# Performance work log

Measured on AMD Instinct MI355X. Metric: run time of the kernel, lower is better.

The kernel has to match this reference:

```python
import jax, jax.numpy as jnp
import numpy as np
import math

VOCAB = 32000
HIDDEN = 256
N_HEADS = 8
HEAD_DIM = 32
MAX_LEN = 2048


def _pos_encoding(max_len, d_model, dtype=jnp.float32):
    # Matches PositionalEncoding buffer (even d_model).
    pos = jnp.arange(max_len, dtype=dtype)[:, None]                       # [L,1]
    div = jnp.exp(jnp.arange(0, d_model, 2, dtype=dtype) * (-(math.log(10000.0) / d_model)))
    ang = pos * div                                                        # [L, d/2]
    pe = jnp.zeros((max_len, d_model), dtype=dtype)
    pe = pe.at[:, 0::2].set(jnp.sin(ang))
    pe = pe.at[:, 1::2].set(jnp.cos(ang))
    return pe


def setup_inputs() -> dict:
    key = jax.random.key(0)
    ks = jax.random.split(key, 7)
    B, S = 8, 2047
    s = 0.02
    x = jax.random.randint(ks[0], (B, S), 0, VOCAB + 1, dtype=jnp.int64)
    emb_w = jax.random.normal(ks[1], (VOCAB + 1, HIDDEN), jnp.float32) * s
    wq = jax.random.normal(ks[2], (N_HEADS, HEAD_DIM, HIDDEN), jnp.float32) * s
    wk = jax.random.normal(ks[3], (N_HEADS, HEAD_DIM, HIDDEN), jnp.float32) * s
    wv = jax.random.normal(ks[4], (N_HEADS, HEAD_DIM, HIDDEN), jnp.float32) * s
    wo = jax.random.normal(ks[5], (HIDDEN, N_HEADS * HEAD_DIM), jnp.float32) * s
    wu = jax.random.normal(ks[6], (VOCAB + 1, HIDDEN), jnp.float32) * s
    return {"x": x, "emb_w": emb_w, "wq": wq, "wk": wk, "wv": wv, "wo": wo, "wu": wu}


def reference(x, emb_w, wq, wk, wv, wo, wu):
    B, S = x.shape
    # prepend CLS token (id=2)
    tok = jnp.concatenate([jnp.full((B, 1), 2, dtype=x.dtype), x], axis=1)  # [B, S+1]
    y = emb_w[tok]                                                          # [B, S+1, H]
    y = y + _pos_encoding(S + 1, HIDDEN, y.dtype)
    # batched per-head QKV (nn.Linear: out = in @ W.T)
    q = jnp.einsum('bsh,nkh->bnsk', y, wq)
    k = jnp.einsum('bsh,nkh->bnsk', y, wk)
    v = jnp.einsum('bsh,nkh->bnsk', y, wv)
    scores = jnp.einsum('bnsk,bntk->bnst', q, k) / (HEAD_DIM ** 0.5)        # [B,N,S+1,S+1]
    A = jax.nn.softmax(scores, axis=-1)
    o = jnp.einsum('bnst,bntk->bnsk', A, v)                                 # [B,N,S+1,K]
    o = jnp.transpose(o, (0, 2, 1, 3)).reshape(B, S + 1, N_HEADS * HEAD_DIM)
    att = o @ wo.T + y     # residual inside MultiHeadAttention
    y = att + y            # second residual in MultiHeadTransformerPosEmb.forward
    out = y[:, 0, :] @ wu.T                                                 # [B, VOCAB+1]
    return out
```

## Files before the change

### kernel.cpp

```cpp
#include <hip/hip_runtime.h>
#include <stdint.h>

#define B_   8
#define S_   2047
#define L_   2048
#define H_   256
#define NH_  8
#define HD_  32
#define V_   32001
#define NCH_ 128
#define TCH_ 16
#define GRID_ 1024
#define BAR_STRIDE_ 2048

__device__ __forceinline__ void ast(float* p, float v) {
    __hip_atomic_store((unsigned int*)p, __float_as_uint(v),
                       __ATOMIC_RELAXED, __HIP_MEMORY_SCOPE_AGENT);
}
__device__ __forceinline__ float ald(const float* p) {
    return __uint_as_float(__hip_atomic_load((const unsigned int*)p,
                           __ATOMIC_RELAXED, __HIP_MEMORY_SCOPE_AGENT));
}
__device__ __forceinline__ unsigned aadd(unsigned* p) {
    return __hip_atomic_fetch_add(p, 1u, __ATOMIC_RELAXED, __HIP_MEMORY_SCOPE_AGENT);
}
__device__ __forceinline__ unsigned aldu(const unsigned* p) {
    return __hip_atomic_load(p, __ATOMIC_RELAXED, __HIP_MEMORY_SCOPE_AGENT);
}
__device__ __forceinline__ void vdrain() {
    asm volatile("s_waitcnt vmcnt(0)" ::: "memory");
}
__device__ __forceinline__ float foldx(float a, int off) {
    return a + __shfl_xor(a, off, 64);
}
__device__ __forceinline__ float sel8(const float a[8], int j) {
    float v = a[0];
    v = (j == 1) ? a[1] : v;
    v = (j == 2) ? a[2] : v;
    v = (j == 3) ? a[3] : v;
    v = (j == 4) ? a[4] : v;
    v = (j == 5) ? a[5] : v;
    v = (j == 6) ? a[6] : v;
    v = (j == 7) ? a[7] : v;
    return v;
}

__global__ __launch_bounds__(256, 4) void mega(const int* __restrict__ x,
                                               const float* __restrict__ emb,
                                               const float* __restrict__ wq,
                                               const float* __restrict__ wk,
                                               const float* __restrict__ wv,
                                               const float* __restrict__ wo,
                                               const float* __restrict__ wu,
                                               float* __restrict__ out,
                                               float* __restrict__ qk,
                                               float* __restrict__ z,
                                               float* __restrict__ obar,
                                               float* __restrict__ ebar,
                                               unsigned int* __restrict__ bars) {
    int bid = blockIdx.x, tid = threadIdx.x;

    __shared__ float smem[4][2056];
    float* smf = &smem[0][0];

    unsigned* qbar = bars;
    unsigned* acnt = bars + BAR_STRIDE_;
    unsigned* zbar = bars + 2 * BAR_STRIDE_;

    if (bid < NH_) {
        int n = bid;
        float* y0l = smem[0];
        float* q0p = smem[1];
        float* q0l = smem[2];
        float v = emb[2 * H_ + tid] + ((tid & 1) ? 1.0f : 0.0f);
        y0l[tid] = v;
        __syncthreads();
        {
            int k = tid >> 3, part = tid & 7;
            const float* w = wq + (n * HD_ + k) * H_ + part * 32;
            const float* yy = y0l + part * 32;
            float acc = 0.f;
#pragma unroll
            for (int j = 0; j < 32; ++j) acc += w[j] * yy[j];
            q0p[k * 8 + part] = acc;
        }
        __syncthreads();
        if (tid < HD_) {
            float s = 0.f;
#pragma unroll
            for (int j = 0; j < 8; ++j) s += q0p[tid * 8 + j];
            q0l[tid] = s;
        }
        __syncthreads();
        float acc = 0.f;
        for (int k = 0; k < HD_; ++k)
            acc += q0l[k] * wk[(n * HD_ + k) * H_ + tid];
        ast(qk + n * H_ + tid, acc * 0.17677669529663687f);
        vdrain();
        __syncthreads();
        if (tid == 0) {
            if (aadd(qbar) == NH_ - 1) {
                for (int i = 0; i < 32; ++i)
                    __hip_atomic_store(qbar + 528 + i * 16, 1u,
                                       __ATOMIC_RELAXED, __HIP_MEMORY_SCOPE_AGENT);
            }
        }
        __syncthreads();
    }

    {
        int b = bid >> 7, c = bid & 127;
        int lane = tid & 63, w = tid >> 6;
        int h0 = lane * 4;
        int t0 = c * TCH_ + w * 4;

        int toks[4];
#pragma unroll
        for (int i = 0; i < 4; ++i) {
            int t = t0 + i;
            toks[i] = (t == 0) ? 2 : x[b * S_ + t - 1];
        }
        float4 evr[4];
#pragma unroll
        for (int i = 0; i < 4; ++i)
            evr[i] = *(const float4*)(emb + (size_t)toks[i] * H_ + h0);
        const float cdiv = 0.07195578414202881f;
        float div0 = __expf(-(float)(lane * 2) * cdiv);
        float div1 = __expf(-(float)(lane * 2 + 1) * cdiv);
        __builtin_amdgcn_sched_barrier(0);

        if (tid == 0) {
            while (aldu(qbar + 528 + (bid & 31) * 16) == 0u)
                __builtin_amdgcn_s_sleep(2);
        }
        __syncthreads();

        for (int i = tid; i < NH_ * H_; i += 256)
            smem[3][i] = ald(qk + i);
        __syncthreads();
        float4 qr[NH_];
#pragma unroll
        for (int n = 0; n < NH_; ++n)
            qr[n] = *(const float4*)&smem[3][n * H_ + h0];
        __syncthreads();

        float4 acc[NH_];
        float es[NH_];
#pragma unroll
        for (int n = 0; n < NH_; ++n) {
            acc[n] = make_float4(0.f, 0.f, 0.f, 0.f);
            es[n] = 0.f;
        }

#pragma unroll
        for (int i = 0; i < 4; ++i) {
            int t = t0 + i;
            float4 ev = evr[i];
            float a0 = (float)t * div0, a1 = (float)t * div1;
            float4 y4;
            y4.x = ev.x + __sinf(a0); y4.y = ev.y + __cosf(a0);
            y4.z = ev.z + __sinf(a1); y4.w = ev.w + __cosf(a1);

            float a[NH_];
#pragma unroll
            for (int n = 0; n < NH_; ++n)
                a[n] = qr[n].x * y4.x + qr[n].y * y4.y + qr[n].z * y4.z + qr[n].w * y4.w;

            float m4[4];
#pragma unroll
            for (int k = 0; k < 4; ++k) {
                float lo = foldx(a[k], 32), hi = foldx(a[k + 4], 32);
                m4[k] = (lane & 32) ? hi : lo;
            }
            float m2[2];
#pragma unroll
            for (int k = 0; k < 2; ++k) {
                float lo = foldx(m4[k], 16), hi = foldx(m4[k + 2], 16);
                m2[k] = (lane & 16) ? hi : lo;
            }
            float lo = foldx(m2[0], 8), hi = foldx(m2[1], 8);
            float m1 = (lane & 8) ? hi : lo;
            m1 = foldx(m1, 4); m1 = foldx(m1, 2); m1 = foldx(m1, 1);
            float e = __expf(m1);

#pragma unroll
            for (int n = 0; n < NH_; ++n) {
                float en = __shfl(e, n * 8, 64);
                acc[n].x += en * y4.x; acc[n].y += en * y4.y;
                acc[n].z += en * y4.z; acc[n].w += en * y4.w;
                es[n] += en;
            }
        }

#pragma unroll
        for (int n = 0; n < NH_; ++n)
            *(float4*)&smem[w][n * H_ + h0] = acc[n];
        if (lane < NH_) smem[w][2048 + lane] = sel8(es, lane);
        __syncthreads();

#pragma unroll
        for (int jj = 0; jj < (NH_ * H_) / 256; ++jj) {
            int j = jj * 256 + tid;
            atomicAdd(obar + b * (NH_ * H_) + j,
                      smem[0][j] + smem[1][j] + smem[2][j] + smem[3][j]);
        }
        if (tid < NH_)
            atomicAdd(ebar + b * NH_ + tid,
                      smem[0][2048 + tid] + smem[1][2048 + tid]
                    + smem[2][2048 + tid] + smem[3][2048 + tid]);
        vdrain();
        __syncthreads();
        if (tid == 0) aadd(acnt);
    }

    if (bid >= 8 && bid < 16) {
        int b = bid - 8;
        if (tid == 0) {
            while (aldu(acnt) < (unsigned)GRID_) __builtin_amdgcn_s_sleep(2);
        }
        __syncthreads();
        float* ybar_l = smf;
        float* o_l    = smf + 2048;
        float* sB     = smf + 2304;
        if (tid < NH_) sB[tid] = 1.0f / ald(ebar + b * NH_ + tid);
        __syncthreads();
        for (int i = tid; i < NH_ * H_; i += 256)
            ybar_l[i] = ald(obar + b * (NH_ * H_) + i) * sB[i >> 8];
        __syncthreads();
        {
            int n = tid >> 5;
            const float* wrow = wv + (size_t)tid * H_;
            const float* yy = ybar_l + n * H_;
            float s = 0.f;
#pragma unroll 16
            for (int j4 = 0; j4 < H_ / 4; ++j4) {
                float4 w4 = *(const float4*)(wrow + j4 * 4);
                s += w4.x * yy[j4 * 4] + w4.y * yy[j4 * 4 + 1]
                   + w4.z * yy[j4 * 4 + 2] + w4.w * yy[j4 * 4 + 3];
            }
            o_l[tid] = s;
        }
        __syncthreads();
        {
            float y0v = emb[2 * H_ + tid] + ((tid & 1) ? 1.0f : 0.0f);
            const float* wrow = wo + (size_t)tid * (NH_ * HD_);
            float s = 0.f;
#pragma unroll 16
            for (int j4 = 0; j4 < (NH_ * HD_) / 4; ++j4) {
                float4 w4 = *(const float4*)(wrow + j4 * 4);
                s += w4.x * o_l[j4 * 4] + w4.y * o_l[j4 * 4 + 1]
                   + w4.z * o_l[j4 * 4 + 2] + w4.w * o_l[j4 * 4 + 3];
            }
            ast(z + b * H_ + tid, s + 2.0f * y0v);
        }
        vdrain();
        __syncthreads();
        if (tid == 0) {
            if (aadd(zbar) == B_ - 1) {
                for (int i = 0; i < 32; ++i)
                    __hip_atomic_store(zbar + 528 + i * 16, 1u,
                                       __ATOMIC_RELAXED, __HIP_MEMORY_SCOPE_AGENT);
            }
        }
        __syncthreads();
    }

    {
        int lane = tid & 63, w = tid >> 6;
        int m = lane & 15, g = lane >> 4;
        int base = bid * 32;

        int rl0 = w * 4 + g;
        int v0 = base + rl0;
        int vc0 = (v0 < V_) ? v0 : (V_ - 1);
        const float* wr0 = wu + (size_t)vc0 * H_ + m * 16;
        float4 p00 = *(const float4*)(wr0);
        float4 p01 = *(const float4*)(wr0 + 4);
        float4 p02 = *(const float4*)(wr0 + 8);
        float4 p03 = *(const float4*)(wr0 + 12);
        __builtin_amdgcn_sched_barrier(0);

        if (tid == 0) {
            while (aldu(zbar + 528 + (bid & 31) * 16) == 0u)
                __builtin_amdgcn_s_sleep(2);
        }
        __syncthreads();

        float* zs = smf;
        float* sm_out = smf + 2560;
        for (int i = tid; i < B_ * H_; i += 256) {
            int bb = i >> 8, h = i & 255;
            zs[bb * 320 + (h >> 4) * 20 + (h & 15)] = ald(z + i);
        }
        __syncthreads();

#pragma unroll
        for (int pass = 0; pass < 2; ++pass) {
            int rl = pass * 16 + w * 4 + g;
            float4 w0, w1, w2, w3;
            if (pass == 0) { w0 = p00; w1 = p01; w2 = p02; w3 = p03; }
            else {
                int v = base + rl;
                int vc = (v < V_) ? v : (V_ - 1);
                const float* wr = wu + (size_t)vc * H_ + m * 16;
                w0 = *(const float4*)(wr);
                w1 = *(const float4*)(wr + 4);
                w2 = *(const float4*)(wr + 8);
                w3 = *(const float4*)(wr + 12);
            }
            float acc[B_];
#pragma unroll
            for (int bb = 0; bb < B_; ++bb) {
                const float* zb = zs + bb * 320 + m * 20;
                float4 z0 = *(const float4*)(zb);
                float4 z1 = *(const float4*)(zb + 4);
                float4 z2 = *(const float4*)(zb + 8);
                float4 z3 = *(const float4*)(zb + 12);
                acc[bb] = z0.x * w0.x + z0.y * w0.y + z0.z * w0.z + z0.w * w0.w
                        + z1.x * w1.x + z1.y * w1.y + z1.z * w1.z + z1.w * w1.w
                        + z2.x * w2.x + z2.y * w2.y + z2.z * w2.z + z2.w * w2.w
                        + z3.x * w3.x + z3.y * w3.y + z3.z * w3.z + z3.w * w3.w;
            }
#pragma unroll
            for (int off = 1; off <= 8; off <<= 1) {
#pragma unroll
                for (int bb = 0; bb < B_; ++bb) acc[bb] += __shfl_xor(acc[bb], off, 64);
            }
            if (m < B_) sm_out[m * 33 + rl] = sel8(acc, m);
        }
        __syncthreads();
        {
            int bb = tid >> 5, vl = tid & 31, vv = base + vl;
            if (vv < V_) out[bb * V_ + vv] = sm_out[bb * 33 + vl];
        }
    }
}

extern "C" void kernel_launch(void* const* d_in, const int* in_sizes, int n_in,
                              void* d_out, int out_size, void* d_ws, size_t ws_size,
                              hipStream_t stream) {
    const int*   x   = (const int*)d_in[0];
    const float* emb = (const float*)d_in[1];
    const float* wq  = (const float*)d_in[2];
    const float* wk  = (const float*)d_in[3];
    const float* wv  = (const float*)d_in[4];
    const float* wo  = (const float*)d_in[5];
    const float* wu  = (const float*)d_in[6];
    float*       out = (float*)d_out;

    float* qk   = (float*)d_ws;
    float* z    = qk + NH_ * H_;
    float* obar = z + B_ * H_;
    float* ebar = obar + B_ * NH_ * H_;
    unsigned int* bars = (unsigned int*)(ebar + B_ * NH_);

    hipMemsetAsync(obar, 0,
                   (B_ * NH_ * H_ + B_ * NH_) * sizeof(float)
                 + 3 * BAR_STRIDE_ * sizeof(unsigned int), stream);

    mega<<<GRID_, 256, 0, stream>>>(x, emb, wq, wk, wv, wo, wu, out,
                                    qk, z, obar, ebar, bars);
}
```

Measured before the change: 160.7 us.

## Replace contended atomic reduction with partial-sum buffers and replicate broadcast vectors

Each attention block now writes its per-block partial sums to a private psum slot instead of doing float atomicAdds into a shared obar. A new grid-wide reduction stage of 512 blocks, gated by an extra barrier, sums those partials. The qk and z broadcast vectors are written as 64 replicas so readers spread across different addresses, and the ebar counters are padded to separate cache lines. The aim is to cut atomic contention and hot-spot reads, at the cost of an extra barrier phase and more global traffic.

```diff
diff --git a/kernel.cpp b/kernel.cpp
--- a/kernel.cpp
+++ b/kernel.cpp
@@ -11,6 +11,7 @@
 #define NCH_ 128
 #define TCH_ 16
 #define GRID_ 1024
+#define NREP_ 64
 #define BAR_STRIDE_ 2048
 
 __device__ __forceinline__ void ast(float* p, float v) {
@@ -53,10 +54,11 @@
                                                const float* __restrict__ wo,
                                                const float* __restrict__ wu,
                                                float* __restrict__ out,
-                                               float* __restrict__ qk,
-                                               float* __restrict__ z,
+                                               float* __restrict__ qk_rep,
+                                               float* __restrict__ z_rep,
+                                               float* __restrict__ psum,
                                                float* __restrict__ obar,
-                                               float* __restrict__ ebar,
+                                               float* __restrict__ ebar_pad,
                                                unsigned int* __restrict__ bars) {
     int bid = blockIdx.x, tid = threadIdx.x;
 
@@ -64,8 +66,9 @@
     float* smf = &smem[0][0];
 
     unsigned* qbar = bars;
-    unsigned* acnt = bars + BAR_STRIDE_;
-    unsigned* zbar = bars + 2 * BAR_STRIDE_;
+    unsigned* abar = bars + BAR_STRIDE_;
+    unsigned* rbar = bars + 2 * BAR_STRIDE_;
+    unsigned* zbar = bars + 3 * BAR_STRIDE_;
 
     if (bid < NH_) {
         int n = bid;
@@ -95,7 +98,9 @@
         float acc = 0.f;
         for (int k = 0; k < HD_; ++k)
             acc += q0l[k] * wk[(n * HD_ + k) * H_ + tid];
-        ast(qk + n * H_ + tid, acc * 0.17677669529663687f);
+        float qv = acc * 0.17677669529663687f;
+        for (int r = 0; r < NREP_; ++r)
+            ast(qk_rep + r * (NH_ * H_) + n * H_ + tid, qv);
         vdrain();
         __syncthreads();
         if (tid == 0) {
@@ -135,8 +140,9 @@
         }
         __syncthreads();
 
+        const float* qsrc = qk_rep + (bid & (NREP_ - 1)) * (NH_ * H_);
         for (int i = tid; i < NH_ * H_; i += 256)
-            smem[3][i] = ald(qk + i);
+            smem[3][i] = ald(qsrc + i);
         __syncthreads();
         float4 qr[NH_];
 #pragma unroll
@@ -201,28 +207,66 @@
 #pragma unroll
         for (int jj = 0; jj < (NH_ * H_) / 256; ++jj) {
             int j = jj * 256 + tid;
-            atomicAdd(obar + b * (NH_ * H_) + j,
-                      smem[0][j] + smem[1][j] + smem[2][j] + smem[3][j]);
+            ast(psum + (size_t)bid * (NH_ * H_) + j,
+                smem[0][j] + smem[1][j] + smem[2][j] + smem[3][j]);
         }
         if (tid < NH_)
-            atomicAdd(ebar + b * NH_ + tid,
+            atomicAdd(ebar_pad + (b * NH_ + tid) * 16,
                       smem[0][2048 + tid] + smem[1][2048 + tid]
                     + smem[2][2048 + tid] + smem[3][2048 + tid]);
         vdrain();
         __syncthreads();
-        if (tid == 0) aadd(acnt);
+        if (tid == 0) {
+            if (aadd(abar) == GRID_ - 1) {
+                for (int i = 0; i < 32; ++i)
+                    __hip_atomic_store(abar + 528 + i * 16, 1u,
+                                       __ATOMIC_RELAXED, __HIP_MEMORY_SCOPE_AGENT);
+            }
+        }
+        __syncthreads();
     }
 
-    if (bid >= 8 && bid < 16) {
-        int b = bid - 8;
-        if (tid == 0) {
-            while (aldu(acnt) < (unsigned)GRID_) __builtin_amdgcn_s_sleep(2);
+    if (bid < 512) {
+        int b = bid >> 6;
+        int j0 = (bid & 63) * 32;
+        if (tid == 0) {
+            while (aldu(abar + 528 + (bid & 31) * 16) == 0u)
+                __builtin_amdgcn_s_sleep(2);
+        }
+        __syncthreads();
+        int jl = tid & 31, cg = tid >> 5;
+        float s = 0.f;
+#pragma unroll 16
+        for (int cc = cg * 16; cc < cg * 16 + 16; ++cc)
+            s += ald(psum + (size_t)(b * NCH_ + cc) * (NH_ * H_) + j0 + jl);
+        smf[jl * 8 + cg] = s;
+        __syncthreads();
+        if (tid < 32) {
+            float t = 0.f;
+#pragma unroll
+            for (int g = 0; g < 8; ++g) t += smf[tid * 8 + g];
+            ast(obar + b * (NH_ * H_) + j0 + tid, t);
+        }
+        vdrain();
+        __syncthreads();
+        if (tid == 0) {
+            if (aadd(rbar) == 511u)
+                __hip_atomic_store(rbar + 528, 1u,
+                                   __ATOMIC_RELAXED, __HIP_MEMORY_SCOPE_AGENT);
+        }
+        __syncthreads();
+    }
+
+    if (bid < B_) {
+        int b = bid;
+        if (tid == 0) {
+            while (aldu(rbar + 528) == 0u) __builtin_amdgcn_s_sleep(2);
         }
         __syncthreads();
         float* ybar_l = smf;
         float* o_l    = smf + 2048;
         float* sB     = smf + 2304;
-        if (tid < NH_) sB[tid] = 1.0f / ald(ebar + b * NH_ + tid);
+        if (tid < NH_) sB[tid] = 1.0f / ald(ebar_pad + (b * NH_ + tid) * 16);
         __syncthreads();
         for (int i = tid; i < NH_ * H_; i += 256)
             ybar_l[i] = ald(obar + b * (NH_ * H_) + i) * sB[i >> 8];
@@ -251,7 +295,9 @@
                 s += w4.x * o_l[j4 * 4] + w4.y * o_l[j4 * 4 + 1]
                    + w4.z * o_l[j4 * 4 + 2] + w4.w * o_l[j4 * 4 + 3];
             }
-            ast(z + b * H_ + tid, s + 2.0f * y0v);
+            float zv = s + 2.0f * y0v;
+            for (int r = 0; r < NREP_; ++r)
+                ast(z_rep + r * (B_ * H_) + b * H_ + tid, zv);
         }
         vdrain();
         __syncthreads();
@@ -286,11 +332,12 @@
         }
         __syncthreads();
 
+        const float* zsrc = z_rep + (bid & (NREP_ - 1)) * (B_ * H_);
         float* zs = smf;
         float* sm_out = smf + 2560;
         for (int i = tid; i < B_ * H_; i += 256) {
             int bb = i >> 8, h = i & 255;
-            zs[bb * 320 + (h >> 4) * 20 + (h & 15)] = ald(z + i);
+            zs[bb * 320 + (h >> 4) * 20 + (h & 15)] = ald(zsrc + i);
         }
         __syncthreads();
 
@@ -348,16 +395,17 @@
     const float* wu  = (const float*)d_in[6];
     float*       out = (float*)d_out;
 
-    float* qk   = (float*)d_ws;
-    float* z    = qk + NH_ * H_;
-    float* obar = z + B_ * H_;
-    float* ebar = obar + B_ * NH_ * H_;
-    unsigned int* bars = (unsigned int*)(ebar + B_ * NH_);
-
-    hipMemsetAsync(obar, 0,
-                   (B_ * NH_ * H_ + B_ * NH_) * sizeof(float)
-                 + 3 * BAR_STRIDE_ * sizeof(unsigned int), stream);
+    float* qk_rep   = (float*)d_ws;
+    float* z_rep    = qk_rep + (size_t)NREP_ * NH_ * H_;
+    float* psum     = z_rep + (size_t)NREP_ * B_ * H_;
+    float* obar     = psum + (size_t)GRID_ * NH_ * H_;
+    float* ebar_pad = obar + B_ * NH_ * H_;
+    unsigned int* bars = (unsigned int*)(ebar_pad + B_ * NH_ * 16);
+
+    hipMemsetAsync(ebar_pad, 0,
+                   B_ * NH_ * 16 * sizeof(float)
+                 + 4 * BAR_STRIDE_ * sizeof(unsigned int), stream);
 
     mega<<<GRID_, 256, 0, stream>>>(x, emb, wq, wk, wv, wo, wu, out,
-                                    qk, z, obar, ebar, bars);
-}
+                                    qk_rep, z_rep, psum, obar, ebar_pad, bars);
+}
```

After: 163.6 us. Within noise of the previous version (+1.8%).
